# Performance work log

Measured on AMD Instinct MI355X. Metric: run time of the kernel, lower is better.

Reference implementation:

```python
import jax, jax.numpy as jnp
import numpy as np

B, T, E, H = 2, 2048, 1024, 16
HD = E // H
EPS = 1e-5


def layer_norm(x, g, b):
    mu = jnp.mean(x, axis=-1, keepdims=True)
    var = jnp.mean(jnp.square(x - mu), axis=-1, keepdims=True)
    return (x - mu) * jax.lax.rsqrt(var + EPS) * g + b


def setup_inputs() -> dict:
    key = jax.random.key(0)
    ks = jax.random.split(key, 12)
    s = 0.02
    return {
        "x": jax.random.normal(ks[0], (B, T, E), jnp.float32),
        "Wk": jax.random.normal(ks[1], (E, E), jnp.float32) * s,
        "Wq": jax.random.normal(ks[2], (E, E), jnp.float32) * s,
        "Wv": jax.random.normal(ks[3], (E, E), jnp.float32) * s,
        "Wp": jax.random.normal(ks[4], (E, E), jnp.float32) * s,
        "bp": jnp.zeros((E,), jnp.float32),
        "W1": jax.random.normal(ks[5], (E, 4 * E), jnp.float32) * s,
        "b1": jnp.zeros((4 * E,), jnp.float32),
        "W2": jax.random.normal(ks[6], (4 * E, E), jnp.float32) * s,
        "b2": jnp.zeros((E,), jnp.float32),
        "g1": jnp.ones((E,), jnp.float32),
        "be1": jnp.zeros((E,), jnp.float32),
        "g2": jnp.ones((E,), jnp.float32),
        "be2": jnp.zeros((E,), jnp.float32),
    }


def reference(x, Wk, Wq, Wv, Wp, bp, W1, b1, W2, b2, g1, be1, g2, be2):
    # --- attention sublayer ---
    h = layer_norm(x, g1, be1)
    q = (h @ Wq).reshape(B, T, H, HD).transpose(0, 2, 1, 3)  # [B,H,T,HD]
    k = (h @ Wk).reshape(B, T, H, HD).transpose(0, 2, 1, 3)
    v = (h @ Wv).reshape(B, T, H, HD).transpose(0, 2, 1, 3)
    scores = jnp.einsum('bhqd,bhkd->bhqk', q, k) * (HD ** -0.5)
    causal = jnp.tril(jnp.ones((T, T), bool))
    scores = jnp.where(causal, scores, -jnp.inf)
    probs = jax.nn.softmax(scores, axis=-1)  # dropout is identity (eval)
    attn = jnp.einsum('bhqk,bhkd->bhqd', probs, v)
    attn = attn.transpose(0, 2, 1, 3).reshape(B, T, E)
    x = x + attn @ Wp + bp
    # --- FFN sublayer ---
    h2 = layer_norm(x, g2, be2)
    ff = jax.nn.relu(h2 @ W1 + b1) @ W2 + b2
    return x + ff
```

## Files before the change

### kernel.cpp

```cpp
#include <hip/hip_runtime.h>
#include <hip/hip_bf16.h>

#define B_ 2
#define T_ 2048
#define E_ 1024
#define H_ 16
#define HD_ 64
#define NT (B_*T_)

typedef __attribute__((ext_vector_type(8))) short s16x8;
typedef __attribute__((ext_vector_type(4))) float f32x4;
typedef __attribute__((ext_vector_type(4))) unsigned int u32x4;

using bf16 = __hip_bfloat16;

#define MFMA16(a,b,c) __builtin_amdgcn_mfma_f32_16x16x32_bf16(a,b,c,0,0,0)

__device__ inline unsigned short f2bf(float f) {
    bf16 h = __float2bfloat16(f);
    return *reinterpret_cast<unsigned short*>(&h);
}

__device__ __forceinline__ unsigned cvt_pk_bf16(float lo, float hi) {
    unsigned r;
    asm("v_cvt_pk_bf16_f32 %0, %1, %2" : "=v"(r) : "v"(lo), "v"(hi));
    return r;
}

__device__ __forceinline__ float exp2_fast(float x) {
    float r;
    asm("v_exp_f32 %0, %1" : "=v"(r) : "v"(x));
    return r;
}

__device__ __forceinline__ void async_cp16(const void* g, void* l) {
    __builtin_amdgcn_global_load_lds((const __attribute__((address_space(1))) void*)g,
                                     (__attribute__((address_space(3))) void*)l,
                                     16, 0, 0);
}

__global__ __launch_bounds__(256) void transpose_all(const float* __restrict__ Wq,
                                                     const float* __restrict__ Wk,
                                                     const float* __restrict__ Wv,
                                                     const float* __restrict__ Wp,
                                                     const float* __restrict__ W1,
                                                     const float* __restrict__ W2,
                                                     bf16* __restrict__ Wqkv_t,
                                                     bf16* __restrict__ W1_t,
                                                     bf16* __restrict__ W2_t) {
    __shared__ float tile[32][33];
    int id = blockIdx.x;
    const float* src; bf16* dst; int K, N, n0, k0;
    float scl = 1.0f;
    if (id < 4096) {
        int z = id >> 10, t = id & 1023;
        src = z == 0 ? Wq : z == 1 ? Wk : z == 2 ? Wv : Wp;
        if (z == 0) scl = 0.125f * 1.44269504088896f;
        dst = Wqkv_t + (size_t)z * 1048576;
        K = 1024; N = 1024; n0 = (t & 31) * 32; k0 = (t >> 5) * 32;
    } else if (id < 8192) {
        int t = id - 4096; src = W1; dst = W1_t; K = 1024; N = 4096;
        n0 = (t & 127) * 32; k0 = (t >> 7) * 32;
    } else {
        int t = id - 8192; src = W2; dst = W2_t; K = 4096; N = 1024;
        n0 = (t & 31) * 32; k0 = (t >> 5) * 32;
    }
    int tx = threadIdx.x, ty = threadIdx.y;
#pragma unroll
    for (int i = 0; i < 4; ++i)
        tile[ty + i*8][tx] = src[(size_t)(k0 + ty + i*8)*N + n0 + tx];
    __syncthreads();
#pragma unroll
    for (int i = 0; i < 4; ++i)
        dst[(size_t)(n0 + ty + i*8)*K + k0 + tx] = __float2bfloat16(tile[tx][ty + i*8] * scl);
}

__global__ __launch_bounds__(256) void ln_kernel(const float* __restrict__ x,
                                                 const float* __restrict__ g,
                                                 const float* __restrict__ b,
                                                 bf16* __restrict__ h) {
    int row = blockIdx.x;
    int tid = threadIdx.x;
    const float4 xv = *reinterpret_cast<const float4*>(x + (size_t)row*E_ + tid*4);
    float s  = xv.x + xv.y + xv.z + xv.w;
    float sq = xv.x*xv.x + xv.y*xv.y + xv.z*xv.z + xv.w*xv.w;
#pragma unroll
    for (int o = 32; o > 0; o >>= 1) { s += __shfl_xor(s, o); sq += __shfl_xor(sq, o); }
    __shared__ float red[8];
    int w = tid >> 6, lane = tid & 63;
    if (lane == 0) { red[w] = s; red[4 + w] = sq; }
    __syncthreads();
    float S = red[0] + red[1] + red[2] + red[3];
    float Q = red[4] + red[5] + red[6] + red[7];
    float mu = S * (1.0f/E_);
    float var = Q * (1.0f/E_) - mu*mu;
    float rs = rsqrtf(var + 1e-5f);
    const float4 gv = *reinterpret_cast<const float4*>(g + tid*4);
    const float4 bv = *reinterpret_cast<const float4*>(b + tid*4);
    ushort4 o4;
    o4.x = f2bf((xv.x - mu)*rs*gv.x + bv.x);
    o4.y = f2bf((xv.y - mu)*rs*gv.y + bv.y);
    o4.z = f2bf((xv.z - mu)*rs*gv.z + bv.z);
    o4.w = f2bf((xv.w - mu)*rs*gv.w + bv.w);
    *reinterpret_cast<ushort4*>(h + (size_t)row*E_ + tid*4) = o4;
}

template<int BM, int BN, int EPI>
__global__ __launch_bounds__(256)
void gemm_t(const bf16* __restrict__ A, const bf16* __restrict__ Bt, void* Cout,
            const float* __restrict__ bias, const float* res,
            int M, int N, int K) {
    constexpr int MT = BM / 32;
    constexpr int NB = BN / 32;
    constexpr int MHALF = BM / 2, NHALF = BN / 2;
    __shared__ bf16 As[BM*64];
    __shared__ bf16 Bs[BN*64];
    int tid = threadIdx.x;
    int lane = tid & 63, w = tid >> 6;
    int wr = w >> 1, wc = w & 1;
    int nbx = gridDim.x;
    int hid = blockIdx.y * nbx + blockIdx.x;
    int cpx = (nbx * gridDim.y) >> 3;
    int nid = (hid & 7) * cpx + (hid >> 3);
    int m0 = (nid / nbx) * BM, n0 = (nid % nbx) * BN;
    int lr = lane & 15, lq = lane >> 4;
    f32x4 acc[MT][NB] = {};
    int srow = w*8 + (lane >> 3);
    int schunk = ((lane & 7) ^ (srow & 7)) * 8;
    const bf16* Ap = A  + (size_t)(m0 + srow)*K + schunk;
    const bf16* Bp = Bt + (size_t)(n0 + srow)*K + schunk;
    for (int k0 = 0; k0 < K; k0 += 64) {
#pragma unroll
        for (int i = 0; i < BM/32; ++i)
            async_cp16(Ap + (size_t)(i*32)*K + k0, (char*)As + i*4096 + w*1024);
#pragma unroll
        for (int i = 0; i < BN/32; ++i)
            async_cp16(Bp + (size_t)(i*32)*K + k0, (char*)Bs + i*4096 + w*1024);
        __syncthreads();
        const char* Asb = (const char*)As;
        const char* Bsb = (const char*)Bs;
        s16x8 af[2][MT], bfr[2][NB];
#pragma unroll
        for (int m = 0; m < MT; ++m) {
            int row = wr*MHALF + m*16 + lr;
            int base = row*128, sw = (row & 7) << 4;
#pragma unroll
            for (int kk = 0; kk < 2; ++kk)
                af[kk][m] = *reinterpret_cast<const s16x8*>(Asb + base + ((kk*64 + lq*16) ^ sw));
        }
#pragma unroll
        for (int n = 0; n < NB; ++n) {
            int row = wc*NHALF + n*16 + lr;
            int base = row*128, sw = (row & 7) << 4;
#pragma unroll
            for (int kk = 0; kk < 2; ++kk)
                bfr[kk][n] = *reinterpret_cast<const s16x8*>(Bsb + base + ((kk*64 + lq*16) ^ sw));
        }
        __builtin_amdgcn_s_setprio(1);
#pragma unroll
        for (int kk = 0; kk < 2; ++kk)
#pragma unroll
            for (int m = 0; m < MT; ++m)
#pragma unroll
                for (int n = 0; n < NB; ++n)
                    acc[m][n] = MFMA16(af[kk][m], bfr[kk][n], acc[m][n]);
        __builtin_amdgcn_s_setprio(0);
        __syncthreads();
    }
#pragma unroll
    for (int m = 0; m < MT; ++m) {
#pragma unroll
        for (int n = 0; n < NB; ++n) {
            int col = n0 + wc*NHALF + n*16 + lr;
#pragma unroll
            for (int r = 0; r < 4; ++r) {
                int row = m0 + wr*MHALF + m*16 + lq*4 + r;
                float v = acc[m][n][r];
                if (EPI == 0) {
                    reinterpret_cast<bf16*>(Cout)[(size_t)row*N + col] = __float2bfloat16(v);
                } else if (EPI == 1) {
                    reinterpret_cast<float*>(Cout)[(size_t)row*N + col] =
                        v + bias[col] + res[(size_t)row*N + col];
                } else {
                    v += bias[col];
                    v = v > 0.f ? v : 0.f;
                    reinterpret_cast<bf16*>(Cout)[(size_t)row*N + col] = __float2bfloat16(v);
                }
            }
        }
    }
}

__global__ __launch_bounds__(256) void v_transpose(const bf16* __restrict__ qkv,
                                                   bf16* __restrict__ Vt) {
    __shared__ unsigned short tile[32][33];
    int tx = threadIdx.x, ty = threadIdx.y;
    int bh = blockIdx.z;
    int b = bh >> 4, h = bh & 15;
    int t0 = blockIdx.x * 32, d0 = blockIdx.y * 32;
    const unsigned short* src = reinterpret_cast<const unsigned short*>(qkv);
#pragma unroll
    for (int i = 0; i < 4; ++i)
        tile[ty + i*8][tx] = src[(size_t)(b*T_ + t0 + ty + i*8)*3072 + 2048 + h*64 + d0 + tx];
    __syncthreads();
    unsigned short* dst = reinterpret_cast<unsigned short*>(Vt);
#pragma unroll
    for (int i = 0; i < 4; ++i)
        dst[(size_t)(bh*64 + d0 + ty + i*8)*T_ + t0 + tx] = tile[tx][ty + i*8];
}

__global__ __launch_bounds__(256)
void flash_attn(const bf16* __restrict__ qkv, const bf16* __restrict__ Vt,
                bf16* __restrict__ O) {
    __shared__ char smem[40960];
    int tid = threadIdx.x;
    int lane = tid & 63, w = tid >> 6;
    int lr = lane & 15, lq = lane >> 4;
    int bh = blockIdx.y, b = bh >> 4, h = bh & 15;
    int pm = (bh & 15) ^ ((bh & 16) ? 31 : 0);
    int qt = (int)(blockIdx.x ^ pm) & 31;
    int q0 = qt * 64;
    int qw = q0 + w * 16;
    const bf16* Qb = qkv + (size_t)(b*T_)*3072 + h*HD_;
    const bf16* Kb = Qb + 1024;
    const bf16* Vb = Vt + (size_t)bh * HD_ * T_;
    char* Pw = smem + 32768 + w*2048;

    int srow_ = w*8 + (lane >> 3);
    int sc_   = (((lane & 7) ^ (srow_ & 7))) * 8;
    const bf16* kS0 = Kb + (size_t)srow_*3072 + sc_;
    const bf16* kS1 = kS0 + (size_t)32*3072;
    const bf16* vS0 = Vb + (size_t)srow_*2048 + sc_;
    const bf16* vS1 = vS0 + (size_t)32*2048;
    char* kD = smem + w*1024;
    char* vD = smem + 16384 + w*1024;

    int sw4 = (lr & 7) << 4;
    int kvo[4], pwo[4];
#pragma unroll
    for (int n = 0; n < 4; ++n) {
        kvo[n] = n*2048 + lr*128 + ((lq << 4) ^ sw4);
        pwo[n] = (lr*128 + n*32 + lq*8) ^ sw4;
    }
    int pao0 = (lr*128 + lq*16) ^ sw4;
    int pao1 = (lr*128 + 64 + lq*16) ^ sw4;

    s16x8 qf[2];
#pragma unroll
    for (int kk = 0; kk < 2; ++kk)
        qf[kk] = *reinterpret_cast<const s16x8*>(Qb + (size_t)(qw + lr)*3072 + kk*32 + lq*8);
    f32x4 od[4] = {};
    const f32x4 Z4 = {0.f, 0.f, 0.f, 0.f};
    float lrun = 0.f;
    int ntiles = qt + 1;

    auto stageNext = [&](int bufi) {
        async_cp16(kS0, kD + bufi*8192);
        async_cp16(kS1, kD + bufi*8192 + 4096);
        async_cp16(vS0, vD + bufi*8192);
        async_cp16(vS1, vD + bufi*8192 + 4096);
        kS0 += 64*3072; kS1 += 64*3072; vS0 += 64; vS1 += 64;
    };

    auto step = [&](const char* Kt, const char* Vtl, bool diag, int kv0) {
        f32x4 sc[4];
        __builtin_amdgcn_s_setprio(1);
#pragma unroll
        for (int n = 0; n < 4; ++n) {
            s16x8 kf0 = *reinterpret_cast<const s16x8*>(Kt + kvo[n]);
            s16x8 kf1 = *reinterpret_cast<const s16x8*>(Kt + (kvo[n] ^ 64));
            f32x4 z = MFMA16(kf0, qf[0], Z4);
            z = MFMA16(kf1, qf[1], z);
            sc[n] = z;
        }
        __builtin_amdgcn_s_setprio(0);
        if (diag) {
            int q = qw + lr;
#pragma unroll
            for (int n = 0; n < 4; ++n)
#pragma unroll
                for (int r = 0; r < 4; ++r)
                    if (kv0 + n*16 + lq*4 + r > q) sc[n][r] = -1e30f;
        }
        float psum = 0.f;
#pragma unroll
        for (int n = 0; n < 4; ++n) {
            float p0 = exp2_fast(sc[n][0]);
            float p1 = exp2_fast(sc[n][1]);
            float p2 = exp2_fast(sc[n][2]);
            float p3 = exp2_fast(sc[n][3]);
            psum += (p0 + p1) + (p2 + p3);
            uint2 pk;
            pk.x = cvt_pk_bf16(p0, p1);
            pk.y = cvt_pk_bf16(p2, p3);
            *reinterpret_cast<uint2*>(Pw + pwo[n]) = pk;
        }
        psum += __shfl_xor(psum, 16);
        psum += __shfl_xor(psum, 32);
        lrun += psum;
        asm volatile("" ::: "memory");
        s16x8 pa0 = *reinterpret_cast<const s16x8*>(Pw + pao0);
        s16x8 pa1 = *reinterpret_cast<const s16x8*>(Pw + pao1);
        __builtin_amdgcn_s_setprio(1);
#pragma unroll
        for (int nd = 0; nd < 4; ++nd) {
            s16x8 vf0 = *reinterpret_cast<const s16x8*>(Vtl + kvo[nd]);
            s16x8 vf1 = *reinterpret_cast<const s16x8*>(Vtl + (kvo[nd] ^ 64));
            od[nd] = MFMA16(pa0, vf0, od[nd]);
            od[nd] = MFMA16(pa1, vf1, od[nd]);
        }
        __builtin_amdgcn_s_setprio(0);
    };

    stageNext(0);
    for (int it = 0; it < ntiles - 1; ++it) {
        int curb = it & 1;
        stageNext(curb ^ 1);
        asm volatile("s_waitcnt vmcnt(4)" ::: "memory");
        __builtin_amdgcn_sched_barrier(0);
        __builtin_amdgcn_s_barrier();
        __builtin_amdgcn_sched_barrier(0);
        step(smem + curb*8192, smem + 16384 + curb*8192, false, 0);
        __builtin_amdgcn_sched_barrier(0);
        __builtin_amdgcn_s_barrier();
        __builtin_amdgcn_sched_barrier(0);
    }
    {
        int curb = (ntiles - 1) & 1;
        asm volatile("s_waitcnt vmcnt(0)" ::: "memory");
        __builtin_amdgcn_sched_barrier(0);
        __builtin_amdgcn_s_barrier();
        __builtin_amdgcn_sched_barrier(0);
        step(smem + curb*8192, smem + 16384 + curb*8192, true, (ntiles - 1) * 64);
    }
    float lR[4];
#pragma unroll
    for (int r = 0; r < 4; ++r) lR[r] = 1.0f / __shfl(lrun, lq*4 + r);
#pragma unroll
    for (int nd = 0; nd < 4; ++nd) {
#pragma unroll
        for (int r = 0; r < 4; ++r) {
            int row = qw + lq*4 + r;
            O[(size_t)(b*T_ + row)*E_ + h*HD_ + nd*16 + lr] = __float2bfloat16(od[nd][r] * lR[r]);
        }
    }
}

extern "C" void kernel_launch(void* const* d_in, const int* in_sizes, int n_in,
                              void* d_out, int out_size, void* d_ws, size_t ws_size,
                              hipStream_t stream) {
    const float* x   = (const float*)d_in[0];
    const float* Wk  = (const float*)d_in[1];
    const float* Wq  = (const float*)d_in[2];
    const float* Wv  = (const float*)d_in[3];
    const float* Wp  = (const float*)d_in[4];
    const float* bp  = (const float*)d_in[5];
    const float* W1  = (const float*)d_in[6];
    const float* b1  = (const float*)d_in[7];
    const float* W2  = (const float*)d_in[8];
    const float* b2  = (const float*)d_in[9];
    const float* g1  = (const float*)d_in[10];
    const float* be1 = (const float*)d_in[11];
    const float* g2  = (const float*)d_in[12];
    const float* be2 = (const float*)d_in[13];
    float* out = (float*)d_out;

    char* ws = (char*)d_ws;
    bf16* Wqkv_t = (bf16*)(ws + 0);
    bf16* Wp_t   = (bf16*)(ws + 6291456);
    bf16* W1_t   = (bf16*)(ws + 8388608);
    bf16* W2_t   = (bf16*)(ws + 16777216);
    bf16* h      = (bf16*)(ws + 25165824);
    bf16* qkv    = (bf16*)(ws + 33554432);
    bf16* Vt     = (bf16*)(ws + 58720256);
    bf16* attnO  = (bf16*)(ws + 67108864);
    bf16* ff1    = (bf16*)(ws + 33554432);
    float* x2    = (ws_size >= 92274688) ? (float*)(ws + 75497472) : out;

    dim3 tb(32, 8);
    transpose_all<<<12288, tb, 0, stream>>>(Wq, Wk, Wv, Wp, W1, W2, Wqkv_t, W1_t, W2_t);

    ln_kernel<<<NT, 256, 0, stream>>>(x, g1, be1, h);
    gemm_t<128,64,0><<<dim3(48, 32), 256, 0, stream>>>(h, Wqkv_t, qkv, nullptr, nullptr, NT, 3072, 1024);
    v_transpose<<<dim3(64, 2, 32), tb, 0, stream>>>(qkv, Vt);
    flash_attn<<<dim3(32, 32), 256, 0, stream>>>(qkv, Vt, attnO);
    gemm_t<64,64,1><<<dim3(16, 64), 256, 0, stream>>>(attnO, Wp_t, x2, bp, x, NT, 1024, 1024);
    ln_kernel<<<NT, 256, 0, stream>>>(x2, g2, be2, h);
    gemm_t<128,64,2><<<dim3(64, 32), 256, 0, stream>>>(h, W1_t, ff1, b1, nullptr, NT, 4096, 1024);
    gemm_t<64,64,1><<<dim3(16, 64), 256, 0, stream>>>(ff1, W2_t, out, b2, x2, NT, 1024, 4096);
}
```

Measured before the change: 211.4 us.

## Add 256x256 eight-wave GEMM with phased async pipeline for QKV and FFN1

Adds a new GEMM kernel with 512 threads and a 256x256 output tile. It double-buffers 128KB of LDS, fills it with async global-to-LDS copies, and splits each K step into four phases that interleave loads with MFMA groups under setprio. It replaces the 128x64 GEMMs for the QKV projection and the first FFN layer, aiming for more data reuse per tile and better overlap of memory with compute. The risks are fewer blocks (192 and 256 against 256 CUs), low occupancy from the large LDS use, and an epilogue that writes scalar, non-vectorised values.

```diff
diff --git a/kernel.cpp b/kernel.cpp
--- a/kernel.cpp
+++ b/kernel.cpp
@@ -10,7 +10,6 @@
 
 typedef __attribute__((ext_vector_type(8))) short s16x8;
 typedef __attribute__((ext_vector_type(4))) float f32x4;
-typedef __attribute__((ext_vector_type(4))) unsigned int u32x4;
 
 using bf16 = __hip_bfloat16;
 
@@ -105,6 +104,120 @@
     *reinterpret_cast<ushort4*>(h + (size_t)row*E_ + tid*4) = o4;
 }
 
+#define RD(p) (*reinterpret_cast<const s16x8*>(p))
+#define MM(m,n) do { acc[m][n] = MFMA16(af[m][0], bfr[n][0], acc[m][n]); \
+                     acc[m][n] = MFMA16(af[m][1], bfr[n][1], acc[m][n]); } while (0)
+#define MFMAS_0 MM(0,0); MM(1,0);
+#define MFMAS_1 MM(2,0); MM(3,0); MM(2,1); MM(3,1); MM(0,1); MM(1,1);
+#define MFMAS_2 MM(4,0); MM(5,0); MM(4,1); MM(5,1); MM(4,2); MM(5,2); \
+                MM(0,2); MM(1,2); MM(2,2); MM(3,2);
+#define MFMAS_3 MM(6,0); MM(7,0); MM(6,1); MM(7,1); MM(6,2); MM(7,2); \
+                MM(6,3); MM(7,3); MM(0,3); MM(1,3); MM(2,3); MM(3,3); \
+                MM(4,3); MM(5,3);
+
+template<int EPI>
+__global__ __launch_bounds__(512)
+void gemm8p(const bf16* __restrict__ A, const bf16* __restrict__ Bt, void* Cout,
+            const float* __restrict__ bias, int M, int N, int K) {
+    __shared__ char smem[131072];
+    int tid = threadIdx.x;
+    int lane = tid & 63, w = tid >> 6;
+    int wm = w >> 2, wn = w & 3;
+    int nbx = gridDim.x;
+    int hid = blockIdx.y * nbx + blockIdx.x;
+    int cpx = (nbx * gridDim.y) >> 3;
+    int nid = (hid & 7) * cpx + (hid >> 3);
+    int m0 = (nid / nbx) * 256, n0 = (nid % nbx) * 256;
+    int lr = lane & 15, lq = lane >> 4;
+    f32x4 acc[8][4] = {};
+    int srow = tid >> 3;
+    int schunk = ((tid & 7) ^ (srow & 7)) * 8;
+    const bf16* ApS = A  + (size_t)(m0 + srow)*K + schunk;
+    const bf16* BpS = Bt + (size_t)(n0 + srow)*K + schunk;
+    int sw4 = (lr & 7) << 4;
+    int x0 = (lq*16) ^ sw4, x1 = (64 + lq*16) ^ sw4;
+    int aoff[8], boff[4];
+#pragma unroll
+    for (int m = 0; m < 8; ++m)
+        aoff[m] = ((m >> 1)*64 + wm*32 + (m & 1)*16 + lr) * 128;
+#pragma unroll
+    for (int n = 0; n < 4; ++n)
+        boff[n] = (n*64 + wn*16 + lr) * 128;
+    int nst = K >> 6;
+    s16x8 af[8][2], bfr[4][2];
+#pragma unroll
+    for (int q = 0; q < 4; ++q) {
+        async_cp16(ApS + (size_t)(q*64)*K, smem + q*8192 + w*1024);
+        async_cp16(BpS + (size_t)(q*64)*K, smem + 32768 + q*8192 + w*1024);
+    }
+    ApS += 64; BpS += 64;
+    asm volatile("s_waitcnt vmcnt(6)" ::: "memory");
+    __builtin_amdgcn_sched_barrier(0);
+    __builtin_amdgcn_s_barrier();
+    __builtin_amdgcn_sched_barrier(0);
+
+#define PHASE(Q) do {                                                              \
+    af[2*Q][0]   = RD(bufA + aoff[2*Q]   + x0);                                    \
+    af[2*Q][1]   = RD(bufA + aoff[2*Q]   + x1);                                    \
+    af[2*Q+1][0] = RD(bufA + aoff[2*Q+1] + x0);                                    \
+    af[2*Q+1][1] = RD(bufA + aoff[2*Q+1] + x1);                                    \
+    bfr[Q][0]    = RD(bufB + boff[Q] + x0);                                        \
+    bfr[Q][1]    = RD(bufB + boff[Q] + x1);                                        \
+    if (more) {                                                                    \
+        async_cp16(ApS + (size_t)(Q*64)*K, stA + Q*8192 + w*1024);                 \
+        async_cp16(BpS + (size_t)(Q*64)*K, stA + 32768 + Q*8192 + w*1024);         \
+        asm volatile("s_waitcnt vmcnt(6)" ::: "memory");                           \
+    } else {                                                                       \
+        if (Q == 0) asm volatile("s_waitcnt vmcnt(4)" ::: "memory");               \
+        else if (Q == 1) asm volatile("s_waitcnt vmcnt(2)" ::: "memory");          \
+        else if (Q == 2) asm volatile("s_waitcnt vmcnt(0)" ::: "memory");          \
+    }                                                                              \
+    __builtin_amdgcn_sched_barrier(0);                                             \
+    __builtin_amdgcn_s_barrier();                                                  \
+    __builtin_amdgcn_sched_barrier(0);                                             \
+    asm volatile("s_waitcnt lgkmcnt(0)" ::: "memory");                             \
+    __builtin_amdgcn_sched_barrier(0);                                             \
+    __builtin_amdgcn_s_setprio(1);                                                 \
+    MFMAS_##Q                                                                      \
+    __builtin_amdgcn_s_setprio(0);                                                 \
+    __builtin_amdgcn_sched_barrier(0);                                             \
+    __builtin_amdgcn_s_barrier();                                                  \
+    __builtin_amdgcn_sched_barrier(0);                                             \
+} while (0)
+
+    for (int t = 0; t < nst; ++t) {
+        const char* bufA = smem + (size_t)(t & 1)*65536;
+        const char* bufB = bufA + 32768;
+        char* stA = smem + (size_t)((t & 1) ^ 1)*65536;
+        bool more = (t + 1 < nst);
+        PHASE(0);
+        PHASE(1);
+        PHASE(2);
+        PHASE(3);
+        ApS += 64; BpS += 64;
+    }
+#undef PHASE
+#pragma unroll
+    for (int m = 0; m < 8; ++m) {
+#pragma unroll
+        for (int n = 0; n < 4; ++n) {
+            int col = n0 + n*64 + wn*16 + lr;
+#pragma unroll
+            for (int r = 0; r < 4; ++r) {
+                int row = m0 + (m >> 1)*64 + wm*32 + (m & 1)*16 + lq*4 + r;
+                float v = acc[m][n][r];
+                if (EPI == 0) {
+                    reinterpret_cast<bf16*>(Cout)[(size_t)row*N + col] = __float2bfloat16(v);
+                } else {
+                    v += bias[col];
+                    v = v > 0.f ? v : 0.f;
+                    reinterpret_cast<bf16*>(Cout)[(size_t)row*N + col] = __float2bfloat16(v);
+                }
+            }
+        }
+    }
+}
+
 template<int BM, int BN, int EPI>
 __global__ __launch_bounds__(256)
 void gemm_t(const bf16* __restrict__ A, const bf16* __restrict__ Bt, void* Cout,
@@ -381,11 +494,11 @@
     transpose_all<<<12288, tb, 0, stream>>>(Wq, Wk, Wv, Wp, W1, W2, Wqkv_t, W1_t, W2_t);
 
     ln_kernel<<<NT, 256, 0, stream>>>(x, g1, be1, h);
-    gemm_t<128,64,0><<<dim3(48, 32), 256, 0, stream>>>(h, Wqkv_t, qkv, nullptr, nullptr, NT, 3072, 1024);
+    gemm8p<0><<<dim3(12, 16), 512, 0, stream>>>(h, Wqkv_t, qkv, nullptr, NT, 3072, 1024);
     v_transpose<<<dim3(64, 2, 32), tb, 0, stream>>>(qkv, Vt);
     flash_attn<<<dim3(32, 32), 256, 0, stream>>>(qkv, Vt, attnO);
     gemm_t<64,64,1><<<dim3(16, 64), 256, 0, stream>>>(attnO, Wp_t, x2, bp, x, NT, 1024, 1024);
     ln_kernel<<<NT, 256, 0, stream>>>(x2, g2, be2, h);
-    gemm_t<128,64,2><<<dim3(64, 32), 256, 0, stream>>>(h, W1_t, ff1, b1, nullptr, NT, 4096, 1024);
+    gemm8p<2><<<dim3(16, 16), 512, 0, stream>>>(h, W1_t, ff1, b1, NT, 4096, 1024);
     gemm_t<64,64,1><<<dim3(16, 64), 256, 0, stream>>>(ff1, W2_t, out, b2, x2, NT, 1024, 4096);
 }
```

Measured after the change: 202.3 us. 1.04x faster.

## Store attention residual in bf16 and shrink QKV/FFN1 GEMM tiles

Applied to the files above, without the earlier changes.

The post-attention residual x2 is now written in bf16 instead of fp32. It is read back by a new bf16 layernorm kernel and by the final GEMM epilogue, which cuts the memory traffic for that intermediate. The QKV and FFN1 GEMMs switch from 128x64 to 64x64 tiles, which doubles the grid size for better CU occupancy at the cost of less data reuse per block. Rounding the residual to bf16 adds error to the residual path.

```diff
diff --git a/kernel.cpp b/kernel.cpp
--- a/kernel.cpp
+++ b/kernel.cpp
@@ -10,7 +10,6 @@
 
 typedef __attribute__((ext_vector_type(8))) short s16x8;
 typedef __attribute__((ext_vector_type(4))) float f32x4;
-typedef __attribute__((ext_vector_type(4))) unsigned int u32x4;
 
 using bf16 = __hip_bfloat16;
 
@@ -19,6 +18,11 @@
 __device__ inline unsigned short f2bf(float f) {
     bf16 h = __float2bfloat16(f);
     return *reinterpret_cast<unsigned short*>(&h);
+}
+
+__device__ __forceinline__ float bf2f(unsigned short u) {
+    unsigned x = ((unsigned)u) << 16;
+    return __uint_as_float(x);
 }
 
 __device__ __forceinline__ unsigned cvt_pk_bf16(float lo, float hi) {
@@ -105,10 +109,41 @@
     *reinterpret_cast<ushort4*>(h + (size_t)row*E_ + tid*4) = o4;
 }
 
+__global__ __launch_bounds__(256) void ln_kernel_b(const bf16* __restrict__ x,
+                                                   const float* __restrict__ g,
+                                                   const float* __restrict__ b,
+                                                   bf16* __restrict__ h) {
+    int row = blockIdx.x;
+    int tid = threadIdx.x;
+    ushort4 u4 = *reinterpret_cast<const ushort4*>(x + (size_t)row*E_ + tid*4);
+    float v0 = bf2f(u4.x), v1 = bf2f(u4.y), v2 = bf2f(u4.z), v3 = bf2f(u4.w);
+    float s  = v0 + v1 + v2 + v3;
+    float sq = v0*v0 + v1*v1 + v2*v2 + v3*v3;
+#pragma unroll
+    for (int o = 32; o > 0; o >>= 1) { s += __shfl_xor(s, o); sq += __shfl_xor(sq, o); }
+    __shared__ float red[8];
+    int w = tid >> 6, lane = tid & 63;
+    if (lane == 0) { red[w] = s; red[4 + w] = sq; }
+    __syncthreads();
+    float S = red[0] + red[1] + red[2] + red[3];
+    float Q = red[4] + red[5] + red[6] + red[7];
+    float mu = S * (1.0f/E_);
+    float var = Q * (1.0f/E_) - mu*mu;
+    float rs = rsqrtf(var + 1e-5f);
+    const float4 gv = *reinterpret_cast<const float4*>(g + tid*4);
+    const float4 bv = *reinterpret_cast<const float4*>(b + tid*4);
+    ushort4 o4;
+    o4.x = f2bf((v0 - mu)*rs*gv.x + bv.x);
+    o4.y = f2bf((v1 - mu)*rs*gv.y + bv.y);
+    o4.z = f2bf((v2 - mu)*rs*gv.z + bv.z);
+    o4.w = f2bf((v3 - mu)*rs*gv.w + bv.w);
+    *reinterpret_cast<ushort4*>(h + (size_t)row*E_ + tid*4) = o4;
+}
+
 template<int BM, int BN, int EPI>
 __global__ __launch_bounds__(256)
 void gemm_t(const bf16* __restrict__ A, const bf16* __restrict__ Bt, void* Cout,
-            const float* __restrict__ bias, const float* res,
+            const float* __restrict__ bias, const void* res,
             int M, int N, int K) {
     constexpr int MT = BM / 32;
     constexpr int NB = BN / 32;
@@ -175,16 +210,25 @@
 #pragma unroll
             for (int r = 0; r < 4; ++r) {
                 int row = m0 + wr*MHALF + m*16 + lq*4 + r;
-                float v = acc[m][n][r];
+                size_t idx = (size_t)row*N + col;
                 if (EPI == 0) {
-                    reinterpret_cast<bf16*>(Cout)[(size_t)row*N + col] = __float2bfloat16(v);
+                    reinterpret_cast<bf16*>(Cout)[idx] = __float2bfloat16(acc[m][n][r]);
+                } else if (EPI == 2) {
+                    float v = acc[m][n][r] + bias[col];
+                    v = v > 0.f ? v : 0.f;
+                    reinterpret_cast<bf16*>(Cout)[idx] = __float2bfloat16(v);
                 } else if (EPI == 1) {
-                    reinterpret_cast<float*>(Cout)[(size_t)row*N + col] =
-                        v + bias[col] + res[(size_t)row*N + col];
+                    float v = acc[m][n][r] + bias[col];
+                    reinterpret_cast<float*>(Cout)[idx] =
+                        v + reinterpret_cast<const float*>(res)[idx];
+                } else if (EPI == 3) {
+                    float v = acc[m][n][r] + bias[col];
+                    reinterpret_cast<bf16*>(Cout)[idx] =
+                        __float2bfloat16(v + reinterpret_cast<const float*>(res)[idx]);
                 } else {
-                    v += bias[col];
-                    v = v > 0.f ? v : 0.f;
-                    reinterpret_cast<bf16*>(Cout)[(size_t)row*N + col] = __float2bfloat16(v);
+                    float v = acc[m][n][r] + bias[col];
+                    reinterpret_cast<float*>(Cout)[idx] =
+                        v + bf2f(reinterpret_cast<const unsigned short*>(res)[idx]);
                 }
             }
         }
@@ -375,17 +419,25 @@
     bf16* Vt     = (bf16*)(ws + 58720256);
     bf16* attnO  = (bf16*)(ws + 67108864);
     bf16* ff1    = (bf16*)(ws + 33554432);
-    float* x2    = (ws_size >= 92274688) ? (float*)(ws + 75497472) : out;
+    bool big = ws_size >= 83886080;
+    bf16* x2b = (bf16*)(ws + 75497472);
 
     dim3 tb(32, 8);
     transpose_all<<<12288, tb, 0, stream>>>(Wq, Wk, Wv, Wp, W1, W2, Wqkv_t, W1_t, W2_t);
 
     ln_kernel<<<NT, 256, 0, stream>>>(x, g1, be1, h);
-    gemm_t<128,64,0><<<dim3(48, 32), 256, 0, stream>>>(h, Wqkv_t, qkv, nullptr, nullptr, NT, 3072, 1024);
+    gemm_t<64,64,0><<<dim3(48, 64), 256, 0, stream>>>(h, Wqkv_t, qkv, nullptr, nullptr, NT, 3072, 1024);
     v_transpose<<<dim3(64, 2, 32), tb, 0, stream>>>(qkv, Vt);
     flash_attn<<<dim3(32, 32), 256, 0, stream>>>(qkv, Vt, attnO);
-    gemm_t<64,64,1><<<dim3(16, 64), 256, 0, stream>>>(attnO, Wp_t, x2, bp, x, NT, 1024, 1024);
-    ln_kernel<<<NT, 256, 0, stream>>>(x2, g2, be2, h);
-    gemm_t<128,64,2><<<dim3(64, 32), 256, 0, stream>>>(h, W1_t, ff1, b1, nullptr, NT, 4096, 1024);
-    gemm_t<64,64,1><<<dim3(16, 64), 256, 0, stream>>>(ff1, W2_t, out, b2, x2, NT, 1024, 4096);
-}
+    if (big) {
+        gemm_t<64,64,3><<<dim3(16, 64), 256, 0, stream>>>(attnO, Wp_t, x2b, bp, x, NT, 1024, 1024);
+        ln_kernel_b<<<NT, 256, 0, stream>>>(x2b, g2, be2, h);
+        gemm_t<64,64,2><<<dim3(64, 64), 256, 0, stream>>>(h, W1_t, ff1, b1, nullptr, NT, 4096, 1024);
+        gemm_t<64,64,4><<<dim3(16, 64), 256, 0, stream>>>(ff1, W2_t, out, b2, x2b, NT, 1024, 4096);
+    } else {
+        gemm_t<64,64,1><<<dim3(16, 64), 256, 0, stream>>>(attnO, Wp_t, out, bp, x, NT, 1024, 1024);
+        ln_kernel<<<NT, 256, 0, stream>>>(out, g2, be2, h);
+        gemm_t<64,64,2><<<dim3(64, 64), 256, 0, stream>>>(h, W1_t, ff1, b1, nullptr, NT, 4096, 1024);
+        gemm_t<64,64,1><<<dim3(16, 64), 256, 0, stream>>>(ff1, W2_t, out, b2, out, NT, 1024, 4096);
+    }
+}
```

New measurement: 239.1 us. 1.13x slower.
